# Kernel tuning notes

Measured on AMD Instinct MI355X. Metric: run time of the kernel, lower is better.

Reference implementation:

```python
import jax, jax.numpy as jnp
import numpy as np

N_NODES = 50000
N_EDGES = 1600000
IN_DIM = 512
OUT_DIM = 256


def setup_inputs() -> dict:
    key = jax.random.key(0)
    k1, k2, k3, k4, k5, k6 = jax.random.split(key, 6)
    inputs = jax.random.normal(k1, (N_NODES, IN_DIM), dtype=jnp.float32)
    edge_row = jax.random.randint(k2, (N_EDGES,), 0, N_NODES, dtype=jnp.int32)
    edge_col = jax.random.randint(k3, (N_EDGES,), 0, N_NODES, dtype=jnp.int32)
    edge_val = jax.random.uniform(k4, (N_EDGES,), dtype=jnp.float32)
    stdv = 1.0 / np.sqrt(OUT_DIM)
    weight = jax.random.uniform(k5, (IN_DIM, OUT_DIM), dtype=jnp.float32, minval=-stdv, maxval=stdv)
    bias = jax.random.uniform(k6, (OUT_DIM,), dtype=jnp.float32, minval=-stdv, maxval=stdv)
    return {"inputs": inputs, "edge_row": edge_row, "edge_col": edge_col,
            "edge_val": edge_val, "weight": weight, "bias": bias}


def reference(inputs, edge_row, edge_col, edge_val, weight, bias):
    # dense GEMM: [N, in] @ [in, out] -> [N, out]
    support = inputs @ weight
    # SpMM: out[r] += val * support[c] for each edge (r, c, val)
    gathered = edge_val[:, None] * support[edge_col]  # [E, out]
    output = jax.ops.segment_sum(gathered, edge_row, num_segments=N_NODES)
    return output + bias
```

## Files before the change

kernel.cpp:

```cpp
#include <hip/hip_runtime.h>

#define N_NODES 50000
#define N_EDGES 1600000
#define IN_DIM 512
#define OUT_DIM 256

#define BM 32
#define BN 256
#define BK 32
#define APAD 8
#define LDA (BK + APAD)

#define RPB   128
#define NBKT  391
#define CHUNK 2048
#define EPT   8
#define CAP   5120

typedef unsigned int u32;
typedef unsigned short u16;
typedef short bf16x8 __attribute__((ext_vector_type(8)));
typedef float f32x4 __attribute__((ext_vector_type(4)));

__device__ __forceinline__ float bf_to_f(u16 u) { return __uint_as_float(((u32)u) << 16); }
__device__ __forceinline__ u16 f_to_bf(float f) {
    u32 u = __float_as_uint(f);
    u32 r = (u + 0x7fffu + ((u >> 16) & 1u)) >> 16;
    return (u16)r;
}

__global__ __launch_bounds__(256) void scatter1(const int* __restrict__ er,
                                                const int* __restrict__ ec,
                                                const float* __restrict__ ev,
                                                int* __restrict__ cursor,
                                                int2* __restrict__ tmp) {
    __shared__ int  hcnt[NBKT];
    __shared__ int  loff[NBKT];
    __shared__ int  gbase[NBKT];
    __shared__ int  sc[512];
    __shared__ int2 estage[CHUNK];
    __shared__ u16  bslot[CHUNK];

    const int t = threadIdx.x;
    const int base = blockIdx.x * CHUNK;
    const int nedge = min(CHUNK, N_EDGES - base);

    for (int k = t; k < NBKT; k += 256) hcnt[k] = 0;
    __syncthreads();

    int w0[EPT], w1[EPT], rk[EPT];
    #pragma unroll
    for (int j = 0; j < EPT; ++j) {
        const int i = j * 256 + t;
        rk[j] = -1;
        if (i < nedge) {
            const int e = base + i;
            const int r = er[e];
            const int bk = r >> 7;
            w0[j] = ec[e] | ((r & 127) << 16) | (bk << 23);
            w1[j] = __float_as_int(ev[e]);
            rk[j] = atomicAdd(&hcnt[bk], 1);
        }
    }
    __syncthreads();

    sc[t]       = (t < NBKT) ? hcnt[t] : 0;
    sc[t + 256] = (t + 256 < NBKT) ? hcnt[t + 256] : 0;
    __syncthreads();
    #pragma unroll
    for (int off = 1; off < 512; off <<= 1) {
        const int a0 = (t >= off) ? sc[t - off] : 0;
        const int a1 = sc[t + 256 - off];
        __syncthreads();
        sc[t] += a0;
        sc[t + 256] += a1;
        __syncthreads();
    }
    if (t < NBKT)       loff[t]       = sc[t] - hcnt[t];
    if (t + 256 < NBKT) loff[t + 256] = sc[t + 256] - hcnt[t + 256];

    if (t < NBKT && hcnt[t] > 0)
        gbase[t] = t * CAP + atomicAdd(&cursor[t], hcnt[t]);
    if (t + 256 < NBKT && hcnt[t + 256] > 0)
        gbase[t + 256] = (t + 256) * CAP + atomicAdd(&cursor[t + 256], hcnt[t + 256]);
    __syncthreads();

    #pragma unroll
    for (int j = 0; j < EPT; ++j) {
        if (rk[j] >= 0) {
            const int bk = ((u32)w0[j]) >> 23;
            const int s = loff[bk] + rk[j];
            estage[s] = make_int2(w0[j], w1[j]);
            bslot[s]  = (u16)bk;
        }
    }
    __syncthreads();

    for (int s = t; s < nedge; s += 256) {
        const int bk = bslot[s];
        const int2 e2 = estage[s];
        const int gpos = gbase[bk] + (s - loff[bk]);
        if (gpos < (bk + 1) * CAP)
            tmp[gpos] = e2;
    }
}

__global__ __launch_bounds__(256) void scatter2(const int* __restrict__ cursor,
                                                const int2* __restrict__ tmp,
                                                int* __restrict__ row_ptr,
                                                int2* __restrict__ sedge) {
    __shared__ int sc[512];
    __shared__ int orig[512];
    __shared__ int rcnt[RPB];
    __shared__ int rsc[RPB];
    __shared__ int rcur[RPB];
    const int t = threadIdx.x;
    const int b = blockIdx.x;

    const int c0 = (t < NBKT) ? min(cursor[t], CAP) : 0;
    const int c1 = (t + 256 < NBKT) ? min(cursor[t + 256], CAP) : 0;
    sc[t] = c0;       orig[t] = c0;
    sc[t + 256] = c1; orig[t + 256] = c1;
    __syncthreads();
    #pragma unroll
    for (int off = 1; off < 512; off <<= 1) {
        const int a0 = (t >= off) ? sc[t - off] : 0;
        const int a1 = sc[t + 256 - off];
        __syncthreads();
        sc[t] += a0;
        sc[t + 256] += a1;
        __syncthreads();
    }
    const int gb = sc[b] - orig[b];
    const int n  = orig[b];
    const int2* src = tmp + (size_t)b * CAP;

    if (b == 0 && t == 0) row_ptr[N_NODES] = N_EDGES;

    if (t < RPB) rcnt[t] = 0;
    __syncthreads();
    for (int i = t; i < n; i += 256)
        atomicAdd(&rcnt[(((u32)src[i].x) >> 16) & 127], 1);
    __syncthreads();

    if (t < RPB) rsc[t] = rcnt[t];
    __syncthreads();
    #pragma unroll
    for (int off = 1; off < RPB; off <<= 1) {
        int a = 0;
        if (t < RPB && t >= off) a = rsc[t - off];
        __syncthreads();
        if (t < RPB) rsc[t] += a;
        __syncthreads();
    }
    if (t < RPB) {
        const int excl = rsc[t] - rcnt[t];
        rcur[t] = gb + excl;
        const int row = b * RPB + t;
        if (row < N_NODES) row_ptr[row] = gb + excl;
    }
    __syncthreads();

    for (int i = t; i < n; i += 256) {
        const int2 e2 = src[i];
        const int rloc = (((u32)e2.x) >> 16) & 127;
        const int pos = atomicAdd(&rcur[rloc], 1);
        sedge[pos] = make_int2(e2.x & 0xFFFF, e2.y);
    }
}

__global__ __launch_bounds__(256) void wcvt_zero(const float* __restrict__ W,
                                                 u16* __restrict__ WT,
                                                 int* __restrict__ cursor) {
    if (blockIdx.x < 2) {
        const int i = blockIdx.x * 256 + threadIdx.x;
        if (i < NBKT) cursor[i] = 0;
    }
    const int n  = threadIdx.x;
    const int k0 = blockIdx.x * 4;
    ushort4 o;
    o.x = f_to_bf(W[(size_t)(k0 + 0) * OUT_DIM + n]);
    o.y = f_to_bf(W[(size_t)(k0 + 1) * OUT_DIM + n]);
    o.z = f_to_bf(W[(size_t)(k0 + 2) * OUT_DIM + n]);
    o.w = f_to_bf(W[(size_t)(k0 + 3) * OUT_DIM + n]);
    *(ushort4*)(WT + (size_t)n * IN_DIM + k0) = o;
}

__global__ __launch_bounds__(256) void gemm_mfma(const float* __restrict__ X,
                                                 const u16* __restrict__ WT,
                                                 u16* __restrict__ Sb) {
    __shared__ u16 As[BM * LDA];
    __shared__ u16 Bs[BN * LDA];

    const int tid  = threadIdx.x;
    const int wave = tid >> 6;
    const int lane = tid & 63;
    const int r0   = blockIdx.x * BM;
    const int wn   = wave * 64;
    const int l15  = lane & 15;
    const int quad = lane >> 4;

    f32x4 acc[2][4];
    #pragma unroll
    for (int i = 0; i < 2; ++i)
        #pragma unroll
        for (int j = 0; j < 4; ++j) acc[i][j] = (f32x4)0.f;

    const int arow = tid >> 3;
    const int akp  = (tid & 7) * 4;
    const int xrow = min(r0 + arow, N_NODES - 1);
    const float* xsrc = X + (size_t)xrow * IN_DIM + akp;
    const int brow = tid >> 1;
    const int bkp  = (tid & 1) * 16;
    const u16* bsrc  = WT + (size_t)brow * IN_DIM + bkp;
    const u16* bsrc2 = bsrc + (size_t)128 * IN_DIM;

    float4 fA0 = *(const float4*)(xsrc + 0);
    uint4  rB0 = *(const uint4*)(bsrc + 0);
    uint4  rB1 = *(const uint4*)(bsrc + 8);
    uint4  rB2 = *(const uint4*)(bsrc2 + 0);
    uint4  rB3 = *(const uint4*)(bsrc2 + 8);

    for (int kc = 0; kc < IN_DIM; kc += BK) {
        {
            ushort4 p0;
            p0.x = f_to_bf(fA0.x); p0.y = f_to_bf(fA0.y); p0.z = f_to_bf(fA0.z); p0.w = f_to_bf(fA0.w);
            *(ushort4*)&As[arow * LDA + akp] = p0;
            *(uint4*)&Bs[brow * LDA + bkp + 0] = rB0;
            *(uint4*)&Bs[brow * LDA + bkp + 8] = rB1;
            *(uint4*)&Bs[(brow + 128) * LDA + bkp + 0] = rB2;
            *(uint4*)&Bs[(brow + 128) * LDA + bkp + 8] = rB3;
        }
        __syncthreads();

        if (kc + BK < IN_DIM) {
            fA0 = *(const float4*)(xsrc + kc + BK);
            rB0 = *(const uint4*)(bsrc + kc + BK + 0);
            rB1 = *(const uint4*)(bsrc + kc + BK + 8);
            rB2 = *(const uint4*)(bsrc2 + kc + BK + 0);
            rB3 = *(const uint4*)(bsrc2 + kc + BK + 8);
        }

        bf16x8 af[2], bfr[4];
        #pragma unroll
        for (int mt = 0; mt < 2; ++mt)
            af[mt] = *(const bf16x8*)&As[(mt * 16 + l15) * LDA + quad * 8];
        #pragma unroll
        for (int nt = 0; nt < 4; ++nt)
            bfr[nt] = *(const bf16x8*)&Bs[(wn + nt * 16 + l15) * LDA + quad * 8];
        #pragma unroll
        for (int mt = 0; mt < 2; ++mt)
            #pragma unroll
            for (int nt = 0; nt < 4; ++nt)
                acc[mt][nt] = __builtin_amdgcn_mfma_f32_16x16x32_bf16(
                    af[mt], bfr[nt], acc[mt][nt], 0, 0, 0);
        __syncthreads();
    }

    #pragma unroll
    for (int mt = 0; mt < 2; ++mt) {
        #pragma unroll
        for (int r = 0; r < 4; ++r) {
            const int grow = r0 + mt * 16 + quad * 4 + r;
            if (grow < N_NODES) {
                u16* dst = Sb + (size_t)grow * OUT_DIM + wn + l15;
                #pragma unroll
                for (int nt = 0; nt < 4; ++nt)
                    dst[nt * 16] = f_to_bf(acc[mt][nt][r]);
            }
        }
    }
}

__global__ __launch_bounds__(256) void csr_spmm(const int* __restrict__ row_ptr,
                                                const int2* __restrict__ sedge,
                                                const u16* __restrict__ Sb,
                                                const float* __restrict__ bias,
                                                float* __restrict__ out,
                                                int rbase) {
    const int wave = threadIdx.x >> 6;
    const int lane = threadIdx.x & 63;
    const int r = rbase + blockIdx.x * 4 + wave;
    if (r >= N_NODES) return;

    const int start = row_ptr[r];
    const int end   = row_ptr[r + 1];

    float4 acc = *(const float4*)(bias + lane * 4);
    const u16* sbase = Sb + lane * 4;

    int e = start;
    for (; e + 16 <= end; e += 16) {
        int2 ed[16];
        #pragma unroll
        for (int j = 0; j < 16; ++j) ed[j] = sedge[e + j];

        ushort4 sv[16];
        #pragma unroll
        for (int j = 0; j < 16; ++j)
            sv[j] = *(const ushort4*)(sbase + (size_t)ed[j].x * OUT_DIM);

        #pragma unroll
        for (int j = 0; j < 16; ++j) {
            const float vj = __int_as_float(ed[j].y);
            acc.x += vj * bf_to_f(sv[j].x);
            acc.y += vj * bf_to_f(sv[j].y);
            acc.z += vj * bf_to_f(sv[j].z);
            acc.w += vj * bf_to_f(sv[j].w);
        }
    }
    if (e < end) {
        int2 ed[16];
        #pragma unroll
        for (int j = 0; j < 16; ++j)
            ed[j] = sedge[min(e + j, end - 1)];
        #pragma unroll
        for (int j = 0; j < 16; ++j)
            if (e + j >= end) ed[j].y = 0;

        ushort4 sv[16];
        #pragma unroll
        for (int j = 0; j < 16; ++j)
            sv[j] = *(const ushort4*)(sbase + (size_t)ed[j].x * OUT_DIM);

        #pragma unroll
        for (int j = 0; j < 16; ++j) {
            const float vj = __int_as_float(ed[j].y);
            acc.x += vj * bf_to_f(sv[j].x);
            acc.y += vj * bf_to_f(sv[j].y);
            acc.z += vj * bf_to_f(sv[j].z);
            acc.w += vj * bf_to_f(sv[j].w);
        }
    }

    *(float4*)(out + (size_t)r * OUT_DIM + lane * 4) = acc;
}

extern "C" void kernel_launch(void* const* d_in, const int* in_sizes, int n_in,
                              void* d_out, int out_size, void* d_ws, size_t ws_size,
                              hipStream_t stream) {
    const float* X    = (const float*)d_in[0];
    const int*   er   = (const int*)d_in[1];
    const int*   ec   = (const int*)d_in[2];
    const float* ev   = (const float*)d_in[3];
    const float* W    = (const float*)d_in[4];
    const float* bias = (const float*)d_in[5];
    float* out        = (float*)d_out;

    char* ws = (char*)d_ws;
    u16*  Sb      = (u16*) (ws);
    int2* tmp     = (int2*)(ws);
    int*  cursor  = (int*) (ws + 16100000);
    int2* sedge   = (int2*)(ws + 25600000);
    u16*  WT      = (u16*) (ws + 38400000);
    int*  row_ptr = (int*) (ws + 38662144);

    hipLaunchKernelGGL(wcvt_zero, dim3(IN_DIM / 4), dim3(256), 0, stream,
                       W, WT, cursor);
    hipLaunchKernelGGL(scatter1, dim3((N_EDGES + CHUNK - 1) / CHUNK), dim3(256), 0,
                       stream, er, ec, ev, cursor, tmp);
    hipLaunchKernelGGL(scatter2, dim3(NBKT), dim3(256), 0, stream,
                       cursor, tmp, row_ptr, sedge);
    hipLaunchKernelGGL(gemm_mfma, dim3((N_NODES + BM - 1) / BM), dim3(256), 0,
                       stream, X, WT, Sb);
    hipLaunchKernelGGL(csr_spmm, dim3(25000 / 4), dim3(256), 0, stream,
                       row_ptr, sedge, Sb, bias, out, 0);
    hipLaunchKernelGGL(csr_spmm, dim3(25000 / 4), dim3(256), 0, stream,
                       row_ptr, sedge, Sb, bias, out, 25000);
}
```

Measured before the change: 391.3 us.

## Replace LDS-staged GEMM with direct-register MFMA loads and enlarge scatter chunks

The GEMM no longer stages tiles in shared memory with barriers. Each wave now loads its A fragments (fp32, converted to bf16 in registers) and its B fragments straight from global memory into MFMA operands, computing a 32x128 tile per wave across a 128-row by 128-column block. This removes the LDS traffic and the syncthreads, at the cost of uncoalesced 32-byte row-strided global loads and more per-lane redundant traffic served from cache. The scatter chunk size and edges per thread are also doubled, which halves the number of scatter1 blocks.

```diff
diff --git a/kernel.cpp b/kernel.cpp
--- a/kernel.cpp
+++ b/kernel.cpp
@@ -5,16 +5,12 @@
 #define IN_DIM 512
 #define OUT_DIM 256
 
-#define BM 32
-#define BN 256
 #define BK 32
-#define APAD 8
-#define LDA (BK + APAD)
 
 #define RPB   128
 #define NBKT  391
-#define CHUNK 2048
-#define EPT   8
+#define CHUNK 4096
+#define EPT   16
 #define CAP   5120
 
 typedef unsigned int u32;
@@ -27,6 +23,15 @@
     u32 u = __float_as_uint(f);
     u32 r = (u + 0x7fffu + ((u >> 16) & 1u)) >> 16;
     return (u16)r;
+}
+
+__device__ __forceinline__ bf16x8 cvt8(float4 a, float4 b) {
+    bf16x8 r;
+    r[0] = (short)f_to_bf(a.x); r[1] = (short)f_to_bf(a.y);
+    r[2] = (short)f_to_bf(a.z); r[3] = (short)f_to_bf(a.w);
+    r[4] = (short)f_to_bf(b.x); r[5] = (short)f_to_bf(b.y);
+    r[6] = (short)f_to_bf(b.z); r[7] = (short)f_to_bf(b.w);
+    return r;
 }
 
 __global__ __launch_bounds__(256) void scatter1(const int* __restrict__ er,
@@ -186,87 +191,56 @@
     *(ushort4*)(WT + (size_t)n * IN_DIM + k0) = o;
 }
 
-__global__ __launch_bounds__(256) void gemm_mfma(const float* __restrict__ X,
-                                                 const u16* __restrict__ WT,
-                                                 u16* __restrict__ Sb) {
-    __shared__ u16 As[BM * LDA];
-    __shared__ u16 Bs[BN * LDA];
-
+__global__ __launch_bounds__(256) void gemm_direct(const float* __restrict__ X,
+                                                   const u16* __restrict__ WT,
+                                                   u16* __restrict__ Sb) {
     const int tid  = threadIdx.x;
     const int wave = tid >> 6;
     const int lane = tid & 63;
-    const int r0   = blockIdx.x * BM;
-    const int wn   = wave * 64;
     const int l15  = lane & 15;
     const int quad = lane >> 4;
-
-    f32x4 acc[2][4];
+    const int rw   = (blockIdx.x >> 1) * 128 + wave * 32;
+    const int c0   = (blockIdx.x & 1) * 128;
+
+    const float* xa0 = X + (size_t)min(rw + l15,      N_NODES - 1) * IN_DIM + quad * 8;
+    const float* xa1 = X + (size_t)min(rw + 16 + l15, N_NODES - 1) * IN_DIM + quad * 8;
+    const u16*   wb  = WT + (size_t)(c0 + l15) * IN_DIM + quad * 8;
+
+    f32x4 acc[2][8];
     #pragma unroll
     for (int i = 0; i < 2; ++i)
         #pragma unroll
-        for (int j = 0; j < 4; ++j) acc[i][j] = (f32x4)0.f;
-
-    const int arow = tid >> 3;
-    const int akp  = (tid & 7) * 4;
-    const int xrow = min(r0 + arow, N_NODES - 1);
-    const float* xsrc = X + (size_t)xrow * IN_DIM + akp;
-    const int brow = tid >> 1;
-    const int bkp  = (tid & 1) * 16;
-    const u16* bsrc  = WT + (size_t)brow * IN_DIM + bkp;
-    const u16* bsrc2 = bsrc + (size_t)128 * IN_DIM;
-
-    float4 fA0 = *(const float4*)(xsrc + 0);
-    uint4  rB0 = *(const uint4*)(bsrc + 0);
-    uint4  rB1 = *(const uint4*)(bsrc + 8);
-    uint4  rB2 = *(const uint4*)(bsrc2 + 0);
-    uint4  rB3 = *(const uint4*)(bsrc2 + 8);
-
+        for (int j = 0; j < 8; ++j) acc[i][j] = (f32x4)0.f;
+
+    #pragma unroll 2
     for (int kc = 0; kc < IN_DIM; kc += BK) {
-        {
-            ushort4 p0;
-            p0.x = f_to_bf(fA0.x); p0.y = f_to_bf(fA0.y); p0.z = f_to_bf(fA0.z); p0.w = f_to_bf(fA0.w);
-            *(ushort4*)&As[arow * LDA + akp] = p0;
-            *(uint4*)&Bs[brow * LDA + bkp + 0] = rB0;
-            *(uint4*)&Bs[brow * LDA + bkp + 8] = rB1;
-            *(uint4*)&Bs[(brow + 128) * LDA + bkp + 0] = rB2;
-            *(uint4*)&Bs[(brow + 128) * LDA + bkp + 8] = rB3;
-        }
-        __syncthreads();
-
-        if (kc + BK < IN_DIM) {
-            fA0 = *(const float4*)(xsrc + kc + BK);
-            rB0 = *(const uint4*)(bsrc + kc + BK + 0);
-            rB1 = *(const uint4*)(bsrc + kc + BK + 8);
-            rB2 = *(const uint4*)(bsrc2 + kc + BK + 0);
-            rB3 = *(const uint4*)(bsrc2 + kc + BK + 8);
-        }
-
-        bf16x8 af[2], bfr[4];
-        #pragma unroll
-        for (int mt = 0; mt < 2; ++mt)
-            af[mt] = *(const bf16x8*)&As[(mt * 16 + l15) * LDA + quad * 8];
-        #pragma unroll
-        for (int nt = 0; nt < 4; ++nt)
-            bfr[nt] = *(const bf16x8*)&Bs[(wn + nt * 16 + l15) * LDA + quad * 8];
-        #pragma unroll
-        for (int mt = 0; mt < 2; ++mt)
-            #pragma unroll
-            for (int nt = 0; nt < 4; ++nt)
-                acc[mt][nt] = __builtin_amdgcn_mfma_f32_16x16x32_bf16(
-                    af[mt], bfr[nt], acc[mt][nt], 0, 0, 0);
-        __syncthreads();
+        const float4 a00 = *(const float4*)(xa0 + kc);
+        const float4 a01 = *(const float4*)(xa0 + kc + 4);
+        const float4 a10 = *(const float4*)(xa1 + kc);
+        const float4 a11 = *(const float4*)(xa1 + kc + 4);
+        bf16x8 bfr[8];
+        #pragma unroll
+        for (int nt = 0; nt < 8; ++nt)
+            bfr[nt] = *(const bf16x8*)(wb + (size_t)nt * 16 * IN_DIM + kc);
+        const bf16x8 af0 = cvt8(a00, a01);
+        const bf16x8 af1 = cvt8(a10, a11);
+        #pragma unroll
+        for (int nt = 0; nt < 8; ++nt) {
+            acc[0][nt] = __builtin_amdgcn_mfma_f32_16x16x32_bf16(af0, bfr[nt], acc[0][nt], 0, 0, 0);
+            acc[1][nt] = __builtin_amdgcn_mfma_f32_16x16x32_bf16(af1, bfr[nt], acc[1][nt], 0, 0, 0);
+        }
     }
 
     #pragma unroll
     for (int mt = 0; mt < 2; ++mt) {
         #pragma unroll
-        for (int r = 0; r < 4; ++r) {
-            const int grow = r0 + mt * 16 + quad * 4 + r;
+        for (int rr = 0; rr < 4; ++rr) {
+            const int grow = rw + mt * 16 + quad * 4 + rr;
             if (grow < N_NODES) {
-                u16* dst = Sb + (size_t)grow * OUT_DIM + wn + l15;
+                u16* dst = Sb + (size_t)grow * OUT_DIM + c0 + l15;
                 #pragma unroll
-                for (int nt = 0; nt < 4; ++nt)
-                    dst[nt * 16] = f_to_bf(acc[mt][nt][r]);
+                for (int nt = 0; nt < 8; ++nt)
+                    dst[nt * 16] = f_to_bf(acc[mt][nt][rr]);
             }
         }
     }
@@ -361,7 +335,7 @@
                        stream, er, ec, ev, cursor, tmp);
     hipLaunchKernelGGL(scatter2, dim3(NBKT), dim3(256), 0, stream,
                        cursor, tmp, row_ptr, sedge);
-    hipLaunchKernelGGL(gemm_mfma, dim3((N_NODES + BM - 1) / BM), dim3(256), 0,
+    hipLaunchKernelGGL(gemm_direct, dim3(2 * ((N_NODES + 127) / 128)), dim3(256), 0,
                        stream, X, WT, Sb);
     hipLaunchKernelGGL(csr_spmm, dim3(25000 / 4), dim3(256), 0, stream,
                        row_ptr, sedge, Sb, bias, out, 0);
```

After: 396.3 us. Within noise of the previous version (+1.3%).
